# Performance work log

Measured on AMD Instinct MI355X. Metric: run time of the kernel, lower is better.

The kernel has to match this reference:

```python
import jax, jax.numpy as jnp
import numpy as np

KERNELSIZE = 9


def generate_pe(pos_num, d_num):
    pos = jnp.arange(pos_num, dtype=jnp.float32)[:, None]
    d_i = jnp.arange(0, d_num + 1, 2, dtype=jnp.float32)[None, :]
    ang = pos / jnp.power(jnp.float32(10000.0), d_i / d_num)  # [pos, ceil((d+1)/2)]
    pe = jnp.zeros((pos_num, d_num), dtype=jnp.float32)
    n_even = pe[:, 0::2].shape[1]
    n_odd = pe[:, 1::2].shape[1]
    pe = pe.at[:, 0::2].set(jnp.sin(ang)[:, :n_even])
    pe = pe.at[:, 1::2].set(jnp.cos(ang)[:, :n_odd])
    return pe


def nearest_idx(in_size, out_size):
    # torch F.interpolate(mode='nearest'): src = floor(dst * in/out)
    return jnp.floor(jnp.arange(out_size) * (in_size / out_size)).astype(jnp.int32)


def setup_inputs() -> dict:
    N, K, C_in, C_out, ks = 30000, 16, 256, 128, KERNELSIZE
    key = jax.random.key(0)
    k0, k1, k2, k3, k4, k5, k6, k7 = jax.random.split(key, 8)
    return {
        "ndata": jax.random.normal(k0, (N, C_in), jnp.float32),
        "neighbors": jax.random.randint(k1, (N, K), 0, N),
        "W_lin": jax.random.normal(k2, (C_out, C_in), jnp.float32) * 0.05,
        "b_lin": jax.random.normal(k3, (C_out,), jnp.float32) * 0.05,
        "weight": jax.random.normal(k4, (C_out, ks), jnp.float32),
        "bias": jax.random.normal(k5, (C_out,), jnp.float32),
        "W_res": jax.random.normal(k6, (C_out, C_in), jnp.float32) * 0.05,
        "b_res": jax.random.normal(k7, (C_out,), jnp.float32) * 0.05,
    }


def reference(ndata, neighbors, W_lin, b_lin, weight, bias, W_res, b_res):
    N = ndata.shape[0]
    C_out, ks = weight.shape
    feat = ndata @ W_lin.T + b_lin                              # [N, D]
    # mailbox = in-neighbor features + self-loop (dgl.add_self_loop)
    mailbox = jnp.concatenate([feat[neighbors], feat[:, None, :]], axis=1)  # [N, S, D]
    S = mailbox.shape[1]
    x = jnp.sort(mailbox, axis=1)                                # sort along neighbor dim
    idx = nearest_idx(ks, S)
    pe = generate_pe(ks, C_out)                                  # [ks, D]
    x = x + pe[idx][None, :, :]                                  # interpolated PE
    w_local = weight[:, idx].T                                   # [S, D] interpolated weight
    Xf = jnp.fft.fft(x, axis=1)
    Wf = jnp.fft.fft(w_local, axis=0)
    y = jnp.fft.ifft(Xf * jnp.conj(Wf)[None, :, :], axis=1).real  # circular correlation
    h = y.sum(axis=1) + bias                                     # [N, D]
    return h + ndata @ W_res.T + b_res
```

## Files before the change

kernel.cpp:

```cpp
#include <hip/hip_runtime.h>
#include <math.h>

#define N_NODES 30000
#define K_NBR   16
#define C_IN    256
#define C_OUT   128
#define KS      9
#define S_MB    17
#define BR      32

typedef __attribute__((ext_vector_type(4))) float f32x4;
typedef __attribute__((ext_vector_type(2))) float f32x2;
typedef __attribute__((ext_vector_type(8))) short bf16x8;

static __device__ __forceinline__ ushort f2bf(float f) {
    uint u = __builtin_bit_cast(uint, f);
    u += 0x7fffu + ((u >> 16) & 1u);
    return (ushort)(u >> 16);
}

__global__ __launch_bounds__(256)
void pcg_prep(const float* __restrict__ W_lin,
              const float* __restrict__ W_res,
              const float* __restrict__ weight,
              const float* __restrict__ b_lin,
              const float* __restrict__ bias,
              const float* __restrict__ b_res,
              ushort* __restrict__ Bf,
              float* __restrict__ Ws,
              float* __restrict__ Cd) {
    if (blockIdx.x == 32) {
        int d = threadIdx.x;
        if (d >= C_OUT) return;
        float freq = powf(10000.0f, -(float)(d & ~1) / (float)C_OUT);
        float ws = 0.f, p = 0.f;
        for (int s = 0; s < S_MB; ++s) {
            int idx = (int)floorf((float)s * (9.0f / 17.0f));
            ws += weight[d * KS + idx];
            float ang = (float)idx * freq;
            p += (d & 1) ? cosf(ang) : sinf(ang);
        }
        Ws[d] = ws;
        Cd[d] = ws * ((float)(K_NBR + 1) * b_lin[d] + p) + bias[d] + b_res[d];
        return;
    }
    const int tt     = blockIdx.x * 256 + threadIdx.x;
    const int col_lo = tt & 15;
    const int ksub   = (tt >> 4) & 3;
    const int colhi  = (tt >> 6) & 15;
    const int kc     = tt >> 10;
    const int col    = colhi * 16 + col_lo;
    const int k0     = kc * 32 + ksub * 8;
    const float* Wr = (col < C_OUT)
        ? &W_lin[(size_t)col * C_IN + k0]
        : &W_res[(size_t)(col - C_OUT) * C_IN + k0];
    const f32x4 w0 = *reinterpret_cast<const f32x4*>(Wr);
    const f32x4 w1 = *reinterpret_cast<const f32x4*>(Wr + 4);
    ushort b[8] = { f2bf(w0.x), f2bf(w0.y), f2bf(w0.z), f2bf(w0.w),
                    f2bf(w1.x), f2bf(w1.y), f2bf(w1.z), f2bf(w1.w) };
    *reinterpret_cast<uint4*>(&Bf[(size_t)tt * 8]) =
        *reinterpret_cast<const uint4*>(b);
}

__global__ __launch_bounds__(256)
void pcg_mfma(const float* __restrict__ ndata,
              const ushort* __restrict__ Bf,
              const float* __restrict__ Ws,
              const float* __restrict__ Cd,
              ushort* __restrict__ Gs,
              ushort* __restrict__ Pc) {
    __shared__ short sA[8192];

    const int t  = threadIdx.x;
    const int n0 = blockIdx.x * BR;

#pragma unroll
    for (int i = 0; i < 4; ++i) {
        const int v    = i * 256 + t;
        const int row  = v >> 5;
        const int kch  = v & 31;
        f32x4 a0 = {0.f, 0.f, 0.f, 0.f}, a1 = {0.f, 0.f, 0.f, 0.f};
        if (n0 + row < N_NODES) {
            const float* p = &ndata[(size_t)(n0 + row) * C_IN + kch * 8];
            a0 = *reinterpret_cast<const f32x4*>(p);
            a1 = *reinterpret_cast<const f32x4*>(p + 4);
        }
        const int kc   = kch >> 2;
        const int ksub = kch & 3;
        const int f    = kc * 2 + (row >> 4);
        const int up   = (((row & 15) | (ksub << 4)) ^ ksub) ^ ((kc & 1) << 2);
        uint4 w;
        w.x = (uint)f2bf(a0.x) | ((uint)f2bf(a0.y) << 16);
        w.y = (uint)f2bf(a0.z) | ((uint)f2bf(a0.w) << 16);
        w.z = (uint)f2bf(a1.x) | ((uint)f2bf(a1.y) << 16);
        w.w = (uint)f2bf(a1.z) | ((uint)f2bf(a1.w) << 16);
        *reinterpret_cast<uint4*>(&sA[f * 512 + up * 8]) = w;
    }
    __syncthreads();

    const int wave = t >> 6;
    const int l    = t & 63;
    const int bu   = l ^ (l >> 4);

    const int ch0 = 2 * wave;
    const int ch1 = 2 * wave + 1;
    const int ch2 = 8 + 2 * wave;
    const int ch3 = 9 + 2 * wave;

    f32x4 acc[2][4] = {};

#pragma unroll
    for (int kc = 0; kc < 8; ++kc) {
        const int ux = bu ^ ((kc & 1) << 2);
        bf16x8 a[2];
#pragma unroll
        for (int rg = 0; rg < 2; ++rg)
            a[rg] = *reinterpret_cast<const bf16x8*>(
                        &sA[(kc * 2 + rg) * 512 + ux * 8]);
        bf16x8 b[4];
        b[0] = *reinterpret_cast<const bf16x8*>(&Bf[((size_t)(kc * 16 + ch0) * 64 + l) * 8]);
        b[1] = *reinterpret_cast<const bf16x8*>(&Bf[((size_t)(kc * 16 + ch1) * 64 + l) * 8]);
        b[2] = *reinterpret_cast<const bf16x8*>(&Bf[((size_t)(kc * 16 + ch2) * 64 + l) * 8]);
        b[3] = *reinterpret_cast<const bf16x8*>(&Bf[((size_t)(kc * 16 + ch3) * 64 + l) * 8]);
#pragma unroll
        for (int rg = 0; rg < 2; ++rg)
#pragma unroll
            for (int cg = 0; cg < 4; ++cg)
                acc[rg][cg] = __builtin_amdgcn_mfma_f32_16x16x32_bf16(
                                  a[rg], b[cg], acc[rg][cg], 0, 0, 0);
    }

    const int cl  = l & 15;
    const int c0  = wave * 32 + cl;
    const int c1  = wave * 32 + 16 + cl;
    const float ws0 = Ws[c0], ws1 = Ws[c1];
    const float cd0 = Cd[c0], cd1 = Cd[c1];
    const int rl  = (l >> 4) * 4;
#pragma unroll
    for (int rg = 0; rg < 2; ++rg) {
#pragma unroll
        for (int j = 0; j < 4; ++j) {
            const int row = n0 + rg * 16 + rl + j;
            if (row < N_NODES) {
                const float gs0 = ws0 * acc[rg][0][j];
                const float gs1 = ws1 * acc[rg][1][j];
                Gs[(size_t)row * C_OUT + c0] = f2bf(gs0);
                Gs[(size_t)row * C_OUT + c1] = f2bf(gs1);
                Pc[(size_t)row * C_OUT + c0] = f2bf(gs0 + acc[rg][2][j] + cd0);
                Pc[(size_t)row * C_OUT + c1] = f2bf(gs1 + acc[rg][3][j] + cd1);
            }
        }
    }
}

__global__ __launch_bounds__(256)
void pcg_gather(const int* __restrict__ neighbors,
                const ushort* __restrict__ Gs,
                const ushort* __restrict__ Pc,
                float* __restrict__ out) {
    __shared__ int snb[64];
    const int t = threadIdx.x;
    if (t < 64) snb[t] = neighbors[(size_t)blockIdx.x * 64 + t];
    __syncthreads();

    const int g = t >> 6;
    const int l = t & 63;
    const int n = blockIdx.x * 4 + g;

    uint p = *reinterpret_cast<const uint*>(&Pc[(size_t)n * C_OUT + 2 * l]);
    float a0 = __builtin_bit_cast(float, p << 16);
    float a1 = __builtin_bit_cast(float, p & 0xffff0000u);

#pragma unroll
    for (int k = 0; k < K_NBR; ++k) {
        const int m = snb[g * 16 + k];
        uint v = *reinterpret_cast<const uint*>(&Gs[(size_t)m * C_OUT + 2 * l]);
        a0 += __builtin_bit_cast(float, v << 16);
        a1 += __builtin_bit_cast(float, v & 0xffff0000u);
    }

    f32x2 o = {a0, a1};
    *reinterpret_cast<f32x2*>(&out[(size_t)n * C_OUT + 2 * l]) = o;
}

extern "C" void kernel_launch(void* const* d_in, const int* in_sizes, int n_in,
                              void* d_out, int out_size, void* d_ws, size_t ws_size,
                              hipStream_t stream) {
    const float* ndata     = (const float*)d_in[0];
    const int*   neighbors = (const int*)  d_in[1];
    const float* W_lin     = (const float*)d_in[2];
    const float* b_lin     = (const float*)d_in[3];
    const float* weight    = (const float*)d_in[4];
    const float* bias      = (const float*)d_in[5];
    const float* W_res     = (const float*)d_in[6];
    const float* b_res     = (const float*)d_in[7];
    float* out = (float*)d_out;

    ushort* Bf = (ushort*)d_ws;
    ushort* Gq = Bf + 65536;
    ushort* Pq = Gq + (size_t)N_NODES * C_OUT;
    float*  Ws = (float*)(Pq + (size_t)N_NODES * C_OUT);
    float*  Cd = Ws + C_OUT;

    pcg_prep<<<33, 256, 0, stream>>>(W_lin, W_res, weight, b_lin, bias, b_res,
                                     Bf, Ws, Cd);
    pcg_mfma<<<(N_NODES + BR - 1) / BR, 256, 0, stream>>>(
        ndata, Bf, Ws, Cd, Gq, Pq);
    pcg_gather<<<N_NODES / 4, 256, 0, stream>>>(neighbors, Gq, Pq, out);
}
```

Before: 39.89 us.

## Fuse prep, MFMA and gather kernels into one cooperative persistent kernel

Merges the three launches (weight prep, bf16 MFMA projection, neighbor gather) into a single cooperative kernel that separates the phases with grid-wide syncs and walks tiles and node groups with grid-stride loops. The aim is to remove the gaps and launch overhead between the three dependent kernels. In exchange it adds two grid barriers, caps the grid at a fixed size based on occupancy, and loses the latency hiding a full oversubscribed grid gives the gather phase.

```diff
diff --git a/kernel.cpp b/kernel.cpp
--- a/kernel.cpp
+++ b/kernel.cpp
@@ -1,5 +1,8 @@
 #include <hip/hip_runtime.h>
+#include <hip/hip_cooperative_groups.h>
 #include <math.h>
+
+namespace cg = cooperative_groups;
 
 #define N_NODES 30000
 #define K_NBR   16
@@ -8,6 +11,8 @@
 #define KS      9
 #define S_MB    17
 #define BR      32
+#define NT      ((N_NODES + BR - 1) / BR)
+#define NG      (N_NODES / 4)
 
 typedef __attribute__((ext_vector_type(4))) float f32x4;
 typedef __attribute__((ext_vector_type(2))) float f32x2;
@@ -19,19 +24,46 @@
     return (ushort)(u >> 16);
 }
 
-__global__ __launch_bounds__(256)
-void pcg_prep(const float* __restrict__ W_lin,
-              const float* __restrict__ W_res,
-              const float* __restrict__ weight,
-              const float* __restrict__ b_lin,
-              const float* __restrict__ bias,
-              const float* __restrict__ b_res,
-              ushort* __restrict__ Bf,
-              float* __restrict__ Ws,
-              float* __restrict__ Cd) {
-    if (blockIdx.x == 32) {
-        int d = threadIdx.x;
-        if (d >= C_OUT) return;
+__global__ __launch_bounds__(256, 4)
+void pcg_fused(const float* __restrict__ ndata,
+               const int* __restrict__ neighbors,
+               const float* __restrict__ W_lin,
+               const float* __restrict__ b_lin,
+               const float* __restrict__ weight,
+               const float* __restrict__ bias,
+               const float* __restrict__ W_res,
+               const float* __restrict__ b_res,
+               ushort* __restrict__ Bf,
+               float* __restrict__ Ws,
+               float* __restrict__ Cd,
+               ushort* __restrict__ Gs,
+               ushort* __restrict__ Pc,
+               float* __restrict__ out) {
+    cg::grid_group grid = cg::this_grid();
+    __shared__ short sA[8192];
+    __shared__ int   snb[64];
+
+    const int t = threadIdx.x;
+
+    if (blockIdx.x < 32) {
+        const int tt     = blockIdx.x * 256 + t;
+        const int col_lo = tt & 15;
+        const int ksub   = (tt >> 4) & 3;
+        const int colhi  = (tt >> 6) & 15;
+        const int kc     = tt >> 10;
+        const int col    = colhi * 16 + col_lo;
+        const int k0     = kc * 32 + ksub * 8;
+        const float* Wr = (col < C_OUT)
+            ? &W_lin[(size_t)col * C_IN + k0]
+            : &W_res[(size_t)(col - C_OUT) * C_IN + k0];
+        const f32x4 w0 = *reinterpret_cast<const f32x4*>(Wr);
+        const f32x4 w1 = *reinterpret_cast<const f32x4*>(Wr + 4);
+        ushort b[8] = { f2bf(w0.x), f2bf(w0.y), f2bf(w0.z), f2bf(w0.w),
+                        f2bf(w1.x), f2bf(w1.y), f2bf(w1.z), f2bf(w1.w) };
+        *reinterpret_cast<uint4*>(&Bf[(size_t)tt * 8]) =
+            *reinterpret_cast<const uint4*>(b);
+    } else if (blockIdx.x == 32 && t < C_OUT) {
+        const int d = t;
         float freq = powf(10000.0f, -(float)(d & ~1) / (float)C_OUT);
         float ws = 0.f, p = 0.f;
         for (int s = 0; s < S_MB; ++s) {
@@ -42,145 +74,116 @@
         }
         Ws[d] = ws;
         Cd[d] = ws * ((float)(K_NBR + 1) * b_lin[d] + p) + bias[d] + b_res[d];
-        return;
     }
-    const int tt     = blockIdx.x * 256 + threadIdx.x;
-    const int col_lo = tt & 15;
-    const int ksub   = (tt >> 4) & 3;
-    const int colhi  = (tt >> 6) & 15;
-    const int kc     = tt >> 10;
-    const int col    = colhi * 16 + col_lo;
-    const int k0     = kc * 32 + ksub * 8;
-    const float* Wr = (col < C_OUT)
-        ? &W_lin[(size_t)col * C_IN + k0]
-        : &W_res[(size_t)(col - C_OUT) * C_IN + k0];
-    const f32x4 w0 = *reinterpret_cast<const f32x4*>(Wr);
-    const f32x4 w1 = *reinterpret_cast<const f32x4*>(Wr + 4);
-    ushort b[8] = { f2bf(w0.x), f2bf(w0.y), f2bf(w0.z), f2bf(w0.w),
-                    f2bf(w1.x), f2bf(w1.y), f2bf(w1.z), f2bf(w1.w) };
-    *reinterpret_cast<uint4*>(&Bf[(size_t)tt * 8]) =
-        *reinterpret_cast<const uint4*>(b);
-}
-
-__global__ __launch_bounds__(256)
-void pcg_mfma(const float* __restrict__ ndata,
-              const ushort* __restrict__ Bf,
-              const float* __restrict__ Ws,
-              const float* __restrict__ Cd,
-              ushort* __restrict__ Gs,
-              ushort* __restrict__ Pc) {
-    __shared__ short sA[8192];
-
-    const int t  = threadIdx.x;
-    const int n0 = blockIdx.x * BR;
-
-#pragma unroll
-    for (int i = 0; i < 4; ++i) {
-        const int v    = i * 256 + t;
-        const int row  = v >> 5;
-        const int kch  = v & 31;
-        f32x4 a0 = {0.f, 0.f, 0.f, 0.f}, a1 = {0.f, 0.f, 0.f, 0.f};
-        if (n0 + row < N_NODES) {
-            const float* p = &ndata[(size_t)(n0 + row) * C_IN + kch * 8];
-            a0 = *reinterpret_cast<const f32x4*>(p);
-            a1 = *reinterpret_cast<const f32x4*>(p + 4);
-        }
-        const int kc   = kch >> 2;
-        const int ksub = kch & 3;
-        const int f    = kc * 2 + (row >> 4);
-        const int up   = (((row & 15) | (ksub << 4)) ^ ksub) ^ ((kc & 1) << 2);
-        uint4 w;
-        w.x = (uint)f2bf(a0.x) | ((uint)f2bf(a0.y) << 16);
-        w.y = (uint)f2bf(a0.z) | ((uint)f2bf(a0.w) << 16);
-        w.z = (uint)f2bf(a1.x) | ((uint)f2bf(a1.y) << 16);
-        w.w = (uint)f2bf(a1.z) | ((uint)f2bf(a1.w) << 16);
-        *reinterpret_cast<uint4*>(&sA[f * 512 + up * 8]) = w;
-    }
-    __syncthreads();
-
-    const int wave = t >> 6;
-    const int l    = t & 63;
-    const int bu   = l ^ (l >> 4);
-
-    const int ch0 = 2 * wave;
-    const int ch1 = 2 * wave + 1;
-    const int ch2 = 8 + 2 * wave;
-    const int ch3 = 9 + 2 * wave;
-
-    f32x4 acc[2][4] = {};
-
-#pragma unroll
-    for (int kc = 0; kc < 8; ++kc) {
-        const int ux = bu ^ ((kc & 1) << 2);
-        bf16x8 a[2];
-#pragma unroll
-        for (int rg = 0; rg < 2; ++rg)
-            a[rg] = *reinterpret_cast<const bf16x8*>(
-                        &sA[(kc * 2 + rg) * 512 + ux * 8]);
-        bf16x8 b[4];
-        b[0] = *reinterpret_cast<const bf16x8*>(&Bf[((size_t)(kc * 16 + ch0) * 64 + l) * 8]);
-        b[1] = *reinterpret_cast<const bf16x8*>(&Bf[((size_t)(kc * 16 + ch1) * 64 + l) * 8]);
-        b[2] = *reinterpret_cast<const bf16x8*>(&Bf[((size_t)(kc * 16 + ch2) * 64 + l) * 8]);
-        b[3] = *reinterpret_cast<const bf16x8*>(&Bf[((size_t)(kc * 16 + ch3) * 64 + l) * 8]);
-#pragma unroll
-        for (int rg = 0; rg < 2; ++rg)
-#pragma unroll
-            for (int cg = 0; cg < 4; ++cg)
-                acc[rg][cg] = __builtin_amdgcn_mfma_f32_16x16x32_bf16(
-                                  a[rg], b[cg], acc[rg][cg], 0, 0, 0);
-    }
-
-    const int cl  = l & 15;
-    const int c0  = wave * 32 + cl;
-    const int c1  = wave * 32 + 16 + cl;
-    const float ws0 = Ws[c0], ws1 = Ws[c1];
-    const float cd0 = Cd[c0], cd1 = Cd[c1];
-    const int rl  = (l >> 4) * 4;
-#pragma unroll
-    for (int rg = 0; rg < 2; ++rg) {
-#pragma unroll
-        for (int j = 0; j < 4; ++j) {
-            const int row = n0 + rg * 16 + rl + j;
-            if (row < N_NODES) {
-                const float gs0 = ws0 * acc[rg][0][j];
-                const float gs1 = ws1 * acc[rg][1][j];
-                Gs[(size_t)row * C_OUT + c0] = f2bf(gs0);
-                Gs[(size_t)row * C_OUT + c1] = f2bf(gs1);
-                Pc[(size_t)row * C_OUT + c0] = f2bf(gs0 + acc[rg][2][j] + cd0);
-                Pc[(size_t)row * C_OUT + c1] = f2bf(gs1 + acc[rg][3][j] + cd1);
-            }
+
+    grid.sync();
+
+    {
+        const int wave = t >> 6;
+        const int l    = t & 63;
+        const int bu   = l ^ (l >> 4);
+        const int ch0 = 2 * wave, ch1 = 2 * wave + 1;
+        const int ch2 = 8 + 2 * wave, ch3 = 9 + 2 * wave;
+        const int cl  = l & 15;
+        const int c0  = wave * 32 + cl;
+        const int c1  = wave * 32 + 16 + cl;
+        const int rl  = (l >> 4) * 4;
+
+        for (int tile = blockIdx.x; tile < NT; tile += gridDim.x) {
+            const int n0 = tile * BR;
+
+#pragma unroll
+            for (int i = 0; i < 4; ++i) {
+                const int v    = i * 256 + t;
+                const int row  = v >> 5;
+                const int kch  = v & 31;
+                f32x4 a0 = {0.f, 0.f, 0.f, 0.f}, a1 = {0.f, 0.f, 0.f, 0.f};
+                if (n0 + row < N_NODES) {
+                    const float* p = &ndata[(size_t)(n0 + row) * C_IN + kch * 8];
+                    a0 = *reinterpret_cast<const f32x4*>(p);
+                    a1 = *reinterpret_cast<const f32x4*>(p + 4);
+                }
+                const int kc   = kch >> 2;
+                const int ksub = kch & 3;
+                const int f    = kc * 2 + (row >> 4);
+                const int up   = (((row & 15) | (ksub << 4)) ^ ksub) ^ ((kc & 1) << 2);
+                uint4 w;
+                w.x = (uint)f2bf(a0.x) | ((uint)f2bf(a0.y) << 16);
+                w.y = (uint)f2bf(a0.z) | ((uint)f2bf(a0.w) << 16);
+                w.z = (uint)f2bf(a1.x) | ((uint)f2bf(a1.y) << 16);
+                w.w = (uint)f2bf(a1.z) | ((uint)f2bf(a1.w) << 16);
+                *reinterpret_cast<uint4*>(&sA[f * 512 + up * 8]) = w;
+            }
+            __syncthreads();
+
+            f32x4 acc[2][4] = {};
+#pragma unroll
+            for (int kc = 0; kc < 8; ++kc) {
+                const int ux = bu ^ ((kc & 1) << 2);
+                bf16x8 a[2];
+#pragma unroll
+                for (int rg = 0; rg < 2; ++rg)
+                    a[rg] = *reinterpret_cast<const bf16x8*>(
+                                &sA[(kc * 2 + rg) * 512 + ux * 8]);
+                bf16x8 b[4];
+                b[0] = *reinterpret_cast<const bf16x8*>(&Bf[((size_t)(kc * 16 + ch0) * 64 + l) * 8]);
+                b[1] = *reinterpret_cast<const bf16x8*>(&Bf[((size_t)(kc * 16 + ch1) * 64 + l) * 8]);
+                b[2] = *reinterpret_cast<const bf16x8*>(&Bf[((size_t)(kc * 16 + ch2) * 64 + l) * 8]);
+                b[3] = *reinterpret_cast<const bf16x8*>(&Bf[((size_t)(kc * 16 + ch3) * 64 + l) * 8]);
+#pragma unroll
+                for (int rg = 0; rg < 2; ++rg)
+#pragma unroll
+                    for (int cg = 0; cg < 4; ++cg)
+                        acc[rg][cg] = __builtin_amdgcn_mfma_f32_16x16x32_bf16(
+                                          a[rg], b[cg], acc[rg][cg], 0, 0, 0);
+            }
+
+            const float ws0 = Ws[c0], ws1 = Ws[c1];
+            const float cd0 = Cd[c0], cd1 = Cd[c1];
+#pragma unroll
+            for (int rg = 0; rg < 2; ++rg) {
+#pragma unroll
+                for (int j = 0; j < 4; ++j) {
+                    const int row = n0 + rg * 16 + rl + j;
+                    if (row < N_NODES) {
+                        const float gs0 = ws0 * acc[rg][0][j];
+                        const float gs1 = ws1 * acc[rg][1][j];
+                        Gs[(size_t)row * C_OUT + c0] = f2bf(gs0);
+                        Gs[(size_t)row * C_OUT + c1] = f2bf(gs1);
+                        Pc[(size_t)row * C_OUT + c0] = f2bf(gs0 + acc[rg][2][j] + cd0);
+                        Pc[(size_t)row * C_OUT + c1] = f2bf(gs1 + acc[rg][3][j] + cd1);
+                    }
+                }
+            }
+            __syncthreads();
         }
     }
-}
-
-__global__ __launch_bounds__(256)
-void pcg_gather(const int* __restrict__ neighbors,
-                const ushort* __restrict__ Gs,
-                const ushort* __restrict__ Pc,
-                float* __restrict__ out) {
-    __shared__ int snb[64];
-    const int t = threadIdx.x;
-    if (t < 64) snb[t] = neighbors[(size_t)blockIdx.x * 64 + t];
-    __syncthreads();
-
-    const int g = t >> 6;
-    const int l = t & 63;
-    const int n = blockIdx.x * 4 + g;
-
-    uint p = *reinterpret_cast<const uint*>(&Pc[(size_t)n * C_OUT + 2 * l]);
-    float a0 = __builtin_bit_cast(float, p << 16);
-    float a1 = __builtin_bit_cast(float, p & 0xffff0000u);
-
-#pragma unroll
-    for (int k = 0; k < K_NBR; ++k) {
-        const int m = snb[g * 16 + k];
-        uint v = *reinterpret_cast<const uint*>(&Gs[(size_t)m * C_OUT + 2 * l]);
-        a0 += __builtin_bit_cast(float, v << 16);
-        a1 += __builtin_bit_cast(float, v & 0xffff0000u);
+
+    grid.sync();
+
+    {
+        const int g = t >> 6;
+        const int l = t & 63;
+        for (int grp = blockIdx.x; grp < NG; grp += gridDim.x) {
+            __syncthreads();
+            if (t < 64) snb[t] = neighbors[(size_t)grp * 64 + t];
+            __syncthreads();
+
+            const int n = grp * 4 + g;
+            uint p = *reinterpret_cast<const uint*>(&Pc[(size_t)n * C_OUT + 2 * l]);
+            float a0 = __builtin_bit_cast(float, p << 16);
+            float a1 = __builtin_bit_cast(float, p & 0xffff0000u);
+#pragma unroll
+            for (int k = 0; k < K_NBR; ++k) {
+                const int m = snb[g * 16 + k];
+                uint v = *reinterpret_cast<const uint*>(&Gs[(size_t)m * C_OUT + 2 * l]);
+                a0 += __builtin_bit_cast(float, v << 16);
+                a1 += __builtin_bit_cast(float, v & 0xffff0000u);
+            }
+            f32x2 o = {a0, a1};
+            *reinterpret_cast<f32x2*>(&out[(size_t)n * C_OUT + 2 * l]) = o;
+        }
     }
-
-    f32x2 o = {a0, a1};
-    *reinterpret_cast<f32x2*>(&out[(size_t)n * C_OUT + 2 * l]) = o;
 }
 
 extern "C" void kernel_launch(void* const* d_in, const int* in_sizes, int n_in,
@@ -202,9 +205,18 @@
     float*  Ws = (float*)(Pq + (size_t)N_NODES * C_OUT);
     float*  Cd = Ws + C_OUT;
 
-    pcg_prep<<<33, 256, 0, stream>>>(W_lin, W_res, weight, b_lin, bias, b_res,
-                                     Bf, Ws, Cd);
-    pcg_mfma<<<(N_NODES + BR - 1) / BR, 256, 0, stream>>>(
-        ndata, Bf, Ws, Cd, Gq, Pq);
-    pcg_gather<<<N_NODES / 4, 256, 0, stream>>>(neighbors, Gq, Pq, out);
+    int nb = 0;
+    hipOccupancyMaxActiveBlocksPerMultiprocessor(&nb, (const void*)pcg_fused,
+                                                 256, 0);
+    if (nb < 1) nb = 1;
+    int grid = nb * 256;
+    if (grid > 960) grid = 960;
+
+    void* args[] = { (void*)&ndata, (void*)&neighbors, (void*)&W_lin,
+                     (void*)&b_lin, (void*)&weight, (void*)&bias,
+                     (void*)&W_res, (void*)&b_res,
+                     (void*)&Bf, (void*)&Ws, (void*)&Cd,
+                     (void*)&Gq, (void*)&Pq, (void*)&out };
+    hipLaunchCooperativeKernel((const void*)pcg_fused, dim3(grid), dim3(256),
+                               args, 0, stream);
 }
```

After: 154.7 us. +287.7%, slower.

## Prefetch B fragments one k-step ahead and use hardware bf16 pack conversion

Applied to the files above, without the earlier changes.

Inside the MFMA k-loop, the B weight fragments for the next k-chunk are now loaded from global memory while the current chunk's MFMAs run, using software double-buffering in registers. Float-to-bf16 conversion switches from manual bit manipulation to the v_cvt_pk_bf16_f32 instruction. A minimum-occupancy hint of 4 blocks is added to launch_bounds. The prefetch adds register pressure, and since the fully unrolled loop may already be scheduled well by the compiler, the gain could be small.

```diff
diff --git a/kernel.cpp b/kernel.cpp
--- a/kernel.cpp
+++ b/kernel.cpp
@@ -9,14 +9,21 @@
 #define S_MB    17
 #define BR      32
 
-typedef __attribute__((ext_vector_type(4))) float f32x4;
-typedef __attribute__((ext_vector_type(2))) float f32x2;
-typedef __attribute__((ext_vector_type(8))) short bf16x8;
+typedef __attribute__((ext_vector_type(4))) float  f32x4;
+typedef __attribute__((ext_vector_type(2))) float  f32x2;
+typedef __attribute__((ext_vector_type(8))) short  bf16x8;
+typedef __attribute__((ext_vector_type(4))) uint   u32x4;
 
 static __device__ __forceinline__ ushort f2bf(float f) {
     uint u = __builtin_bit_cast(uint, f);
     u += 0x7fffu + ((u >> 16) & 1u);
     return (ushort)(u >> 16);
+}
+
+static __device__ __forceinline__ uint cvtpk(float a, float b) {
+    uint r;
+    asm("v_cvt_pk_bf16_f32 %0, %1, %2" : "=v"(r) : "v"(a), "v"(b));
+    return r;
 }
 
 __global__ __launch_bounds__(256)
@@ -33,15 +40,16 @@
         int d = threadIdx.x;
         if (d >= C_OUT) return;
         float freq = powf(10000.0f, -(float)(d & ~1) / (float)C_OUT);
-        float ws = 0.f, p = 0.f;
+        float ws = 0.f, pe = 0.f;
         for (int s = 0; s < S_MB; ++s) {
             int idx = (int)floorf((float)s * (9.0f / 17.0f));
             ws += weight[d * KS + idx];
             float ang = (float)idx * freq;
-            p += (d & 1) ? cosf(ang) : sinf(ang);
+            pe += (d & 1) ? cosf(ang) : sinf(ang);
         }
         Ws[d] = ws;
-        Cd[d] = ws * ((float)(K_NBR + 1) * b_lin[d] + p) + bias[d] + b_res[d];
+        Cd[d] = ws * ((float)(K_NBR + 1) * b_lin[d] + pe)
+                + bias[d] + b_res[d];
         return;
     }
     const int tt     = blockIdx.x * 256 + threadIdx.x;
@@ -56,13 +64,16 @@
         : &W_res[(size_t)(col - C_OUT) * C_IN + k0];
     const f32x4 w0 = *reinterpret_cast<const f32x4*>(Wr);
     const f32x4 w1 = *reinterpret_cast<const f32x4*>(Wr + 4);
-    ushort b[8] = { f2bf(w0.x), f2bf(w0.y), f2bf(w0.z), f2bf(w0.w),
-                    f2bf(w1.x), f2bf(w1.y), f2bf(w1.z), f2bf(w1.w) };
-    *reinterpret_cast<uint4*>(&Bf[(size_t)tt * 8]) =
-        *reinterpret_cast<const uint4*>(b);
-}
-
-__global__ __launch_bounds__(256)
+    u32x4 b;
+    b.x = cvtpk(w0.x, w0.y); b.y = cvtpk(w0.z, w0.w);
+    b.z = cvtpk(w1.x, w1.y); b.w = cvtpk(w1.z, w1.w);
+    *reinterpret_cast<u32x4*>(&Bf[(size_t)tt * 8]) = b;
+}
+
+#define LDB(KC, CH) (*reinterpret_cast<const bf16x8*>( \
+        &Bf[((size_t)((KC) * 16 + (CH)) * 64 + l) * 8]))
+
+__global__ __launch_bounds__(256, 4)
 void pcg_mfma(const float* __restrict__ ndata,
               const ushort* __restrict__ Bf,
               const float* __restrict__ Ws,
@@ -89,12 +100,12 @@
         const int ksub = kch & 3;
         const int f    = kc * 2 + (row >> 4);
         const int up   = (((row & 15) | (ksub << 4)) ^ ksub) ^ ((kc & 1) << 2);
-        uint4 w;
-        w.x = (uint)f2bf(a0.x) | ((uint)f2bf(a0.y) << 16);
-        w.y = (uint)f2bf(a0.z) | ((uint)f2bf(a0.w) << 16);
-        w.z = (uint)f2bf(a1.x) | ((uint)f2bf(a1.y) << 16);
-        w.w = (uint)f2bf(a1.z) | ((uint)f2bf(a1.w) << 16);
-        *reinterpret_cast<uint4*>(&sA[f * 512 + up * 8]) = w;
+        u32x4 w;
+        w.x = cvtpk(a0.x, a0.y);
+        w.y = cvtpk(a0.z, a0.w);
+        w.z = cvtpk(a1.x, a1.y);
+        w.w = cvtpk(a1.z, a1.w);
+        *reinterpret_cast<u32x4*>(&sA[f * 512 + up * 8]) = w;
     }
     __syncthreads();
 
@@ -109,25 +120,30 @@
 
     f32x4 acc[2][4] = {};
 
+    bf16x8 b0 = LDB(0, ch0), b1 = LDB(0, ch1);
+    bf16x8 b2 = LDB(0, ch2), b3 = LDB(0, ch3);
+
 #pragma unroll
     for (int kc = 0; kc < 8; ++kc) {
+        bf16x8 p0, p1, p2, p3;
+        if (kc < 7) {
+            p0 = LDB(kc + 1, ch0); p1 = LDB(kc + 1, ch1);
+            p2 = LDB(kc + 1, ch2); p3 = LDB(kc + 1, ch3);
+        }
         const int ux = bu ^ ((kc & 1) << 2);
-        bf16x8 a[2];
-#pragma unroll
-        for (int rg = 0; rg < 2; ++rg)
-            a[rg] = *reinterpret_cast<const bf16x8*>(
-                        &sA[(kc * 2 + rg) * 512 + ux * 8]);
-        bf16x8 b[4];
-        b[0] = *reinterpret_cast<const bf16x8*>(&Bf[((size_t)(kc * 16 + ch0) * 64 + l) * 8]);
-        b[1] = *reinterpret_cast<const bf16x8*>(&Bf[((size_t)(kc * 16 + ch1) * 64 + l) * 8]);
-        b[2] = *reinterpret_cast<const bf16x8*>(&Bf[((size_t)(kc * 16 + ch2) * 64 + l) * 8]);
-        b[3] = *reinterpret_cast<const bf16x8*>(&Bf[((size_t)(kc * 16 + ch3) * 64 + l) * 8]);
-#pragma unroll
-        for (int rg = 0; rg < 2; ++rg)
-#pragma unroll
-            for (int cg = 0; cg < 4; ++cg)
-                acc[rg][cg] = __builtin_amdgcn_mfma_f32_16x16x32_bf16(
-                                  a[rg], b[cg], acc[rg][cg], 0, 0, 0);
+        const bf16x8 a0 = *reinterpret_cast<const bf16x8*>(
+                              &sA[(kc * 2 + 0) * 512 + ux * 8]);
+        const bf16x8 a1 = *reinterpret_cast<const bf16x8*>(
+                              &sA[(kc * 2 + 1) * 512 + ux * 8]);
+        acc[0][0] = __builtin_amdgcn_mfma_f32_16x16x32_bf16(a0, b0, acc[0][0], 0, 0, 0);
+        acc[1][0] = __builtin_amdgcn_mfma_f32_16x16x32_bf16(a1, b0, acc[1][0], 0, 0, 0);
+        acc[0][1] = __builtin_amdgcn_mfma_f32_16x16x32_bf16(a0, b1, acc[0][1], 0, 0, 0);
+        acc[1][1] = __builtin_amdgcn_mfma_f32_16x16x32_bf16(a1, b1, acc[1][1], 0, 0, 0);
+        acc[0][2] = __builtin_amdgcn_mfma_f32_16x16x32_bf16(a0, b2, acc[0][2], 0, 0, 0);
+        acc[1][2] = __builtin_amdgcn_mfma_f32_16x16x32_bf16(a1, b2, acc[1][2], 0, 0, 0);
+        acc[0][3] = __builtin_amdgcn_mfma_f32_16x16x32_bf16(a0, b3, acc[0][3], 0, 0, 0);
+        acc[1][3] = __builtin_amdgcn_mfma_f32_16x16x32_bf16(a1, b3, acc[1][3], 0, 0, 0);
+        if (kc < 7) { b0 = p0; b1 = p1; b2 = p2; b3 = p3; }
     }
 
     const int cl  = l & 15;
```

Result: slower. 41.24 us (+3.4%).
